# Performance work log

Hardware: AMD Instinct MI355X
Metric: run time of the kernel (lower is better)

## Reference

```python
import jax, jax.numpy as jnp
import numpy as np

B, N, M, LDIM, RDIM, AGG = 4, 512, 512, 512, 512, 256


def setup_inputs() -> dict:
    key = jax.random.key(0)
    ks = jax.random.split(key, 7)
    data = jax.random.normal(ks[0], (B, N, LDIM), dtype=jnp.float32)
    crit = jax.random.normal(ks[1], (B, M, RDIM), dtype=jnp.float32)
    Wl = jax.random.normal(ks[2], (LDIM, AGG), dtype=jnp.float32) / np.sqrt(LDIM)
    bl = jax.random.normal(ks[3], (AGG,), dtype=jnp.float32) * 0.01
    Wr = jax.random.normal(ks[4], (RDIM, AGG), dtype=jnp.float32) / np.sqrt(RDIM)
    br = jax.random.normal(ks[5], (AGG,), dtype=jnp.float32) * 0.01
    agg = jax.random.uniform(ks[6], (AGG,), dtype=jnp.float32, minval=-0.01, maxval=0.01)
    return {"data": data, "crit": crit, "Wl": Wl, "bl": bl, "Wr": Wr, "br": br, "agg": agg}


def reference(data, crit, Wl, bl, Wr, br, agg):
    # linear projections
    datalin = jnp.einsum('bnl,la->bna', data, Wl) + bl   # [B,N,A]
    critlin = jnp.einsum('bmr,ra->bma', crit, Wr) + br   # [B,M,A]
    # broadcast add -> tanh -> reduce with agg vector: [B,N,M]
    linsum = jnp.tanh(datalin[:, :, None, :] + critlin[:, None, :, :])  # [B,N,M,A]
    dists = jnp.einsum('bnma,a->bnm', linsum, agg)
    return dists
```

## Files before the change

### kernel.cpp

```cpp
#include <hip/hip_runtime.h>


#define A_DIM 256
#define K_DIM 512
#define NROWS 2048

typedef unsigned short ushort;
typedef __attribute__((ext_vector_type(4))) unsigned short us4;
typedef __attribute__((ext_vector_type(8))) unsigned short us8;
typedef __attribute__((ext_vector_type(8))) short short8;
typedef __attribute__((ext_vector_type(4))) float f32x4;

__device__ inline ushort f2bf(float x) {
    union { float f; unsigned u; } v; v.f = x;
    unsigned r = v.u + 0x7FFFu + ((v.u >> 16) & 1u);
    return (ushort)(r >> 16);
}
__device__ inline float bf2f(ushort h) {
    union { unsigned u; float f; } v; v.u = ((unsigned)h) << 16; return v.f;
}
__device__ inline unsigned pack2bf(float lo, float hi) {
    return (unsigned)f2bf(lo) | ((unsigned)f2bf(hi) << 16);
}

__global__ __launch_bounds__(256) void transpose_w_kernel(
    const float* __restrict__ Wl, const float* __restrict__ Wr,
    ushort* __restrict__ wt)
{
    __shared__ float tile[64][68];
    const int t   = threadIdx.x;
    const int bid = blockIdx.x;
    const int at  = bid & 3;
    const int kt  = (bid >> 2) & 7;
    const int src = bid >> 5;
    const int a0 = at * 64, k0 = kt * 64;
    const float* W = src ? Wr : Wl;
    ushort* out = wt + (size_t)src * (A_DIM * K_DIM);

    const int c4 = (t & 15) * 4;
    const int kr = t >> 4;
#pragma unroll
    for (int r = 0; r < 4; r++) {
        const int k = kr + r * 16;
        *(float4*)&tile[k][c4] = *(const float4*)(W + (size_t)(k0 + k) * A_DIM + a0 + c4);
    }
    __syncthreads();
    const int aL  = t & 63;
    const int ks0 = (t >> 6) * 16;
#pragma unroll
    for (int g = 0; g < 4; g++) {
        us4 o;
#pragma unroll
        for (int i = 0; i < 4; i++) o[i] = f2bf(tile[ks0 + g * 4 + i][aL]);
        *(us4*)(out + (size_t)(a0 + aL) * K_DIM + k0 + ks0 + g * 4) = o;
    }
}

__global__ __launch_bounds__(256) void proj_mfma_kernel(
    const float* __restrict__ data, const float* __restrict__ crit,
    const float* __restrict__ bl, const float* __restrict__ br,
    const ushort* __restrict__ wt, ushort* __restrict__ eplanes)
{
    __shared__ ushort Ws[64][264];

    const int t   = threadIdx.x;
    const int bid = blockIdx.x;
    const int ct  = bid & 3;
    const int rt  = bid >> 2;
    const int src = rt >> 6;
    const int lr0 = (rt & 63) * 32;
    const int c0  = ct * 64;

    const float* X    = src ? crit : data;
    const float* bias = src ? br : bl;
    const ushort* Wt  = wt + (size_t)src * (A_DIM * K_DIM);
    ushort* E = eplanes + (size_t)src * ((size_t)A_DIM * NROWS);

    const int lane = t & 63;
    const int wid  = t >> 6;
    const int wm   = wid >> 1, wn = wid & 1;
    const int quad = lane >> 4, l16 = lane & 15;

    const float* xrow = X + (size_t)(lr0 + wm * 16 + l16) * K_DIM + quad * 8;
    const int aloc0 = wn * 32 + l16;

    f32x4 acc0 = {0.f, 0.f, 0.f, 0.f}, acc1 = {0.f, 0.f, 0.f, 0.f};

    float4 pa = *(const float4*)(xrow);
    float4 pb = *(const float4*)(xrow + 4);

    for (int kc = 0; kc < 2; kc++) {
        __syncthreads();
        {
            const int a  = t & 63;
            const int ks = (t >> 6) * 64;
            const ushort* s = Wt + (size_t)(c0 + a) * K_DIM + kc * 256 + ks;
#pragma unroll
            for (int i = 0; i < 8; i++)
                *(us8*)&Ws[a][ks + i * 8] = *(const us8*)(s + i * 8);
        }
        __syncthreads();

#pragma unroll
        for (int ls = 0; ls < 8; ls++) {
            const int s = kc * 8 + ls;
            float4 ca = pa, cb = pb;
            if (s < 15) {
                pa = *(const float4*)(xrow + (s + 1) * 32);
                pb = *(const float4*)(xrow + (s + 1) * 32 + 4);
            }
            union { short8 s8; unsigned u[4]; } af;
            af.u[0] = pack2bf(ca.x, ca.y);
            af.u[1] = pack2bf(ca.z, ca.w);
            af.u[2] = pack2bf(cb.x, cb.y);
            af.u[3] = pack2bf(cb.z, cb.w);
            short8 b0 = *(const short8*)&Ws[aloc0     ][ls * 32 + quad * 8];
            short8 b1 = *(const short8*)&Ws[aloc0 + 16][ls * 32 + quad * 8];
            acc0 = __builtin_amdgcn_mfma_f32_16x16x32_bf16(af.s8, b0, acc0, 0, 0, 0);
            acc1 = __builtin_amdgcn_mfma_f32_16x16x32_bf16(af.s8, b1, acc1, 0, 0, 0);
        }
    }

    const float c2 = 2.8853900817779268f;
    const int a_col0 = c0 + wn * 32 + l16;
    const int a_col1 = a_col0 + 16;
    const int row0   = lr0 + wm * 16 + quad * 4;
    const float bv0 = bias[a_col0], bv1 = bias[a_col1];
    us4 e0, e1;
#pragma unroll
    for (int i = 0; i < 4; i++) {
        float v0 = (acc0[i] + bv0) * c2;
        float v1 = (acc1[i] + bv1) * c2;
        v0 = fminf(fmaxf(v0, -15.f), 15.f);
        v1 = fminf(fmaxf(v1, -15.f), 15.f);
        e0[i] = f2bf(__builtin_amdgcn_exp2f(v0));
        e1[i] = f2bf(__builtin_amdgcn_exp2f(v1));
    }
    *(us4*)(E + (size_t)a_col0 * NROWS + row0) = e0;
    *(us4*)(E + (size_t)a_col1 * NROWS + row0) = e1;
}

__global__ __launch_bounds__(512) void tanh_reduce_kernel(
    const ushort* __restrict__ eplanes, const float* __restrict__ agg,
    float* __restrict__ out)
{
    __shared__ __align__(16) float et [2][64][68];
    __shared__ __align__(16) float ect[2][64][68];
    __shared__ float aggs[256];

    const int t  = threadIdx.x;
    const int h  = t >> 8;
    const int u  = t & 255;
    const int m0 = blockIdx.x * 64;
    const int n0 = blockIdx.y * 64;
    const int b  = blockIdx.z;

    const size_t PLANE = (size_t)A_DIM * NROWS;
    const ushort* Ed = eplanes;
    const ushort* Ec = eplanes + PLANE;
    const int row_n = b * 512 + n0;
    const int row_m = b * 512 + m0;

    const int tx = u & 15;
    const int ty = u >> 4;

    if (t < 256) aggs[t] = 2.0f * agg[t];

    float acc[4][4];
#pragma unroll
    for (int i = 0; i < 4; i++)
#pragma unroll
        for (int j = 0; j < 4; j++) acc[i][j] = 0.f;
    float sagg = 0.f;

    const int aL = u >> 2;
    const int qd = u & 3;

    float (*eth)[68]  = et[h];
    float (*ecth)[68] = ect[h];

    for (int ch = 0; ch < 2; ch++) {
        const int a0 = h * 128 + ch * 64;
        __syncthreads();
#pragma unroll
        for (int r = 0; r < 4; r++) {
            const int seg = qd * 16 + r * 4;
            us4 d = *(const us4*)(Ed + (size_t)(a0 + aL) * NROWS + row_n + seg);
            us4 c = *(const us4*)(Ec + (size_t)(a0 + aL) * NROWS + row_m + seg);
            float4 ev, cv;
            ev.x = bf2f(d[0]); ev.y = bf2f(d[1]); ev.z = bf2f(d[2]); ev.w = bf2f(d[3]);
            cv.x = bf2f(c[0]); cv.y = bf2f(c[1]); cv.z = bf2f(c[2]); cv.w = bf2f(c[3]);
            *(float4*)&eth [aL][seg] = ev;
            *(float4*)&ecth[aL][seg] = cv;
        }
        __syncthreads();

        for (int p = 0; p < 32; p++) {
            const float2 ag = *(const float2*)&aggs[h * 128 + ch * 64 + p * 2];
            sagg += ag.x + ag.y;
            float4 e0 = *(const float4*)&eth [p * 2 + 0][ty * 4];
            float4 e1 = *(const float4*)&eth [p * 2 + 1][ty * 4];
            float4 f0 = *(const float4*)&ecth[p * 2 + 0][tx * 4];
            float4 f1 = *(const float4*)&ecth[p * 2 + 1][tx * 4];
            const float ea0[4] = {e0.x, e0.y, e0.z, e0.w};
            const float ea1[4] = {e1.x, e1.y, e1.z, e1.w};
            const float fa0[4] = {f0.x, f0.y, f0.z, f0.w};
            const float fa1[4] = {f1.x, f1.y, f1.z, f1.w};
#pragma unroll
            for (int i = 0; i < 4; i++)
#pragma unroll
                for (int j = 0; j < 4; j++) {
                    float q0 = fmaf(ea0[i], fa0[j], 1.f);
                    float q1 = fmaf(ea1[i], fa1[j], 1.f);
                    acc[i][j] = fmaf(fmaf(ag.x, q1, ag.y * q0),
                                     __builtin_amdgcn_rcpf(q0 * q1), acc[i][j]);
                }
        }
    }

    const float base = 0.5f * sagg;
    float* xb = (float*)ect;
    __syncthreads();
    if (h == 1) {
#pragma unroll
        for (int i = 0; i < 4; i++)
#pragma unroll
            for (int j = 0; j < 4; j++)
                xb[u * 17 + i * 4 + j] = base - acc[i][j];
    }
    __syncthreads();
    if (h == 0) {
#pragma unroll
        for (int i = 0; i < 4; i++) {
            float4 v;
            v.x = (base - acc[i][0]) + xb[u * 17 + i * 4 + 0];
            v.y = (base - acc[i][1]) + xb[u * 17 + i * 4 + 1];
            v.z = (base - acc[i][2]) + xb[u * 17 + i * 4 + 2];
            v.w = (base - acc[i][3]) + xb[u * 17 + i * 4 + 3];
            *(float4*)(out + ((size_t)(b * 512 + n0 + ty * 4 + i) * 512) + m0 + tx * 4) = v;
        }
    }
}

extern "C" void kernel_launch(void* const* d_in, const int* in_sizes, int n_in,
                              void* d_out, int out_size, void* d_ws, size_t ws_size,
                              hipStream_t stream) {
    const float* data = (const float*)d_in[0];
    const float* crit = (const float*)d_in[1];
    const float* Wl   = (const float*)d_in[2];
    const float* bl   = (const float*)d_in[3];
    const float* Wr   = (const float*)d_in[4];
    const float* br   = (const float*)d_in[5];
    const float* agg  = (const float*)d_in[6];
    float* out = (float*)d_out;

    ushort* ws16 = (ushort*)d_ws;
    ushort* eplanes = ws16;
    ushort* wt      = ws16 + 2 * (size_t)A_DIM * NROWS;

    transpose_w_kernel<<<dim3(64), 256, 0, stream>>>(Wl, Wr, wt);

    proj_mfma_kernel<<<dim3(512), 256, 0, stream>>>(data, crit, bl, br, wt, eplanes);

    tanh_reduce_kernel<<<dim3(8, 8, 4), 512, 0, stream>>>(eplanes, agg, out);
}
```

Baseline: 110.3 us.

## Group four tanh terms per reciprocal, packed FMA math, prefetch next chunk

The inner tanh-reduce loop now combines four aggregate dimensions into a single rational expression, so only one reciprocal is needed per four tanh terms instead of one per two, and uses packed two-wide FP32 FMAs. It also prefetches the second chunk's bf16 planes into registers while the first chunk is computed, and switches the output and workspace writes to nontemporal stores. Multiplying four (1+e*f) factors risks overflow or precision loss when the exponentials are large, and the extra prefetch registers may lower occupancy.

Measured after the change: 107.8 us. 1.02x faster.

```diff
diff --git a/kernel.cpp b/kernel.cpp
--- a/kernel.cpp
+++ b/kernel.cpp
@@ -10,6 +10,7 @@
 typedef __attribute__((ext_vector_type(8))) unsigned short us8;
 typedef __attribute__((ext_vector_type(8))) short short8;
 typedef __attribute__((ext_vector_type(4))) float f32x4;
+typedef __attribute__((ext_vector_type(2))) float f32x2;
 
 __device__ inline ushort f2bf(float x) {
     union { float f; unsigned u; } v; v.f = x;
@@ -21,6 +22,9 @@
 }
 __device__ inline unsigned pack2bf(float lo, float hi) {
     return (unsigned)f2bf(lo) | ((unsigned)f2bf(hi) << 16);
+}
+__device__ inline f32x2 fma2(f32x2 a, f32x2 b, f32x2 c) {
+    return __builtin_elementwise_fma(a, b, c);
 }
 
 __global__ __launch_bounds__(256) void transpose_w_kernel(
@@ -52,7 +56,7 @@
         us4 o;
 #pragma unroll
         for (int i = 0; i < 4; i++) o[i] = f2bf(tile[ks0 + g * 4 + i][aL]);
-        *(us4*)(out + (size_t)(a0 + aL) * K_DIM + k0 + ks0 + g * 4) = o;
+        __builtin_nontemporal_store(o, (us4*)(out + (size_t)(a0 + aL) * K_DIM + k0 + ks0 + g * 4));
     }
 }
 
@@ -136,8 +140,8 @@
         e0[i] = f2bf(__builtin_amdgcn_exp2f(v0));
         e1[i] = f2bf(__builtin_amdgcn_exp2f(v1));
     }
-    *(us4*)(E + (size_t)a_col0 * NROWS + row0) = e0;
-    *(us4*)(E + (size_t)a_col1 * NROWS + row0) = e1;
+    __builtin_nontemporal_store(e0, (us4*)(E + (size_t)a_col0 * NROWS + row0));
+    __builtin_nontemporal_store(e1, (us4*)(E + (size_t)a_col1 * NROWS + row0));
 }
 
 __global__ __launch_bounds__(512) void tanh_reduce_kernel(
@@ -146,7 +150,7 @@
 {
     __shared__ __align__(16) float et [2][64][68];
     __shared__ __align__(16) float ect[2][64][68];
-    __shared__ float aggs[256];
+    __shared__ __align__(16) float aggs[256];
 
     const int t  = threadIdx.x;
     const int h  = t >> 8;
@@ -166,11 +170,9 @@
 
     if (t < 256) aggs[t] = 2.0f * agg[t];
 
-    float acc[4][4];
-#pragma unroll
-    for (int i = 0; i < 4; i++)
-#pragma unroll
-        for (int j = 0; j < 4; j++) acc[i][j] = 0.f;
+    f32x2 acc2[4][2];
+#pragma unroll
+    for (int i = 0; i < 4; i++) { acc2[i][0] = (f32x2)0.f; acc2[i][1] = (f32x2)0.f; }
     float sagg = 0.f;
 
     const int aL = u >> 2;
@@ -179,41 +181,67 @@
     float (*eth)[68]  = et[h];
     float (*ecth)[68] = ect[h];
 
+    us4 pn[4], pm[4];
+#pragma unroll
+    for (int r = 0; r < 4; r++) {
+        const size_t base = (size_t)(h * 128 + aL) * NROWS;
+        pn[r] = *(const us4*)(Ed + base + row_n + qd * 16 + r * 4);
+        pm[r] = *(const us4*)(Ec + base + row_m + qd * 16 + r * 4);
+    }
+
     for (int ch = 0; ch < 2; ch++) {
-        const int a0 = h * 128 + ch * 64;
         __syncthreads();
 #pragma unroll
         for (int r = 0; r < 4; r++) {
-            const int seg = qd * 16 + r * 4;
-            us4 d = *(const us4*)(Ed + (size_t)(a0 + aL) * NROWS + row_n + seg);
-            us4 c = *(const us4*)(Ec + (size_t)(a0 + aL) * NROWS + row_m + seg);
             float4 ev, cv;
-            ev.x = bf2f(d[0]); ev.y = bf2f(d[1]); ev.z = bf2f(d[2]); ev.w = bf2f(d[3]);
-            cv.x = bf2f(c[0]); cv.y = bf2f(c[1]); cv.z = bf2f(c[2]); cv.w = bf2f(c[3]);
-            *(float4*)&eth [aL][seg] = ev;
-            *(float4*)&ecth[aL][seg] = cv;
-        }
-        __syncthreads();
-
-        for (int p = 0; p < 32; p++) {
-            const float2 ag = *(const float2*)&aggs[h * 128 + ch * 64 + p * 2];
-            sagg += ag.x + ag.y;
-            float4 e0 = *(const float4*)&eth [p * 2 + 0][ty * 4];
-            float4 e1 = *(const float4*)&eth [p * 2 + 1][ty * 4];
-            float4 f0 = *(const float4*)&ecth[p * 2 + 0][tx * 4];
-            float4 f1 = *(const float4*)&ecth[p * 2 + 1][tx * 4];
-            const float ea0[4] = {e0.x, e0.y, e0.z, e0.w};
-            const float ea1[4] = {e1.x, e1.y, e1.z, e1.w};
-            const float fa0[4] = {f0.x, f0.y, f0.z, f0.w};
-            const float fa1[4] = {f1.x, f1.y, f1.z, f1.w};
+            ev.x = bf2f(pn[r][0]); ev.y = bf2f(pn[r][1]);
+            ev.z = bf2f(pn[r][2]); ev.w = bf2f(pn[r][3]);
+            cv.x = bf2f(pm[r][0]); cv.y = bf2f(pm[r][1]);
+            cv.z = bf2f(pm[r][2]); cv.w = bf2f(pm[r][3]);
+            *(float4*)&eth [aL][qd * 16 + r * 4] = ev;
+            *(float4*)&ecth[aL][qd * 16 + r * 4] = cv;
+        }
+        __syncthreads();
+        if (ch == 0) {
+            const size_t base = (size_t)(h * 128 + 64 + aL) * NROWS;
+#pragma unroll
+            for (int r = 0; r < 4; r++) {
+                pn[r] = *(const us4*)(Ed + base + row_n + qd * 16 + r * 4);
+                pm[r] = *(const us4*)(Ec + base + row_m + qd * 16 + r * 4);
+            }
+        }
+
+        for (int qg = 0; qg < 16; qg++) {
+            const float4 ag = *(const float4*)&aggs[h * 128 + ch * 64 + qg * 4];
+            sagg += (ag.x + ag.y) + (ag.z + ag.w);
+            float  en[4][4];
+            f32x2  fm[4][2];
+#pragma unroll
+            for (int v = 0; v < 4; v++) {
+                float4 e4 = *(const float4*)&eth [qg * 4 + v][ty * 4];
+                float4 f4 = *(const float4*)&ecth[qg * 4 + v][tx * 4];
+                en[v][0] = e4.x; en[v][1] = e4.y; en[v][2] = e4.z; en[v][3] = e4.w;
+                fm[v][0] = f32x2{f4.x, f4.y};
+                fm[v][1] = f32x2{f4.z, f4.w};
+            }
 #pragma unroll
             for (int i = 0; i < 4; i++)
 #pragma unroll
-                for (int j = 0; j < 4; j++) {
-                    float q0 = fmaf(ea0[i], fa0[j], 1.f);
-                    float q1 = fmaf(ea1[i], fa1[j], 1.f);
-                    acc[i][j] = fmaf(fmaf(ag.x, q1, ag.y * q0),
-                                     __builtin_amdgcn_rcpf(q0 * q1), acc[i][j]);
+                for (int jp = 0; jp < 2; jp++) {
+                    const f32x2 one = (f32x2)1.f;
+                    f32x2 q0 = fma2((f32x2)en[0][i], fm[0][jp], one);
+                    f32x2 q1 = fma2((f32x2)en[1][i], fm[1][jp], one);
+                    f32x2 q2 = fma2((f32x2)en[2][i], fm[2][jp], one);
+                    f32x2 q3 = fma2((f32x2)en[3][i], fm[3][jp], one);
+                    f32x2 q01 = q0 * q1, q23 = q2 * q3;
+                    f32x2 n01 = fma2((f32x2)ag.x, q1, (f32x2)ag.y * q0);
+                    f32x2 n23 = fma2((f32x2)ag.z, q3, (f32x2)ag.w * q2);
+                    f32x2 N   = fma2(n01, q23, n23 * q01);
+                    f32x2 D   = q01 * q23;
+                    f32x2 r;
+                    r.x = __builtin_amdgcn_rcpf(D.x);
+                    r.y = __builtin_amdgcn_rcpf(D.y);
+                    acc2[i][jp] = fma2(N, r, acc2[i][jp]);
                 }
         }
     }
@@ -225,19 +253,22 @@
 #pragma unroll
         for (int i = 0; i < 4; i++)
 #pragma unroll
-            for (int j = 0; j < 4; j++)
-                xb[u * 17 + i * 4 + j] = base - acc[i][j];
+            for (int jp = 0; jp < 2; jp++) {
+                xb[u * 17 + i * 4 + jp * 2 + 0] = base - acc2[i][jp].x;
+                xb[u * 17 + i * 4 + jp * 2 + 1] = base - acc2[i][jp].y;
+            }
     }
     __syncthreads();
     if (h == 0) {
 #pragma unroll
         for (int i = 0; i < 4; i++) {
-            float4 v;
-            v.x = (base - acc[i][0]) + xb[u * 17 + i * 4 + 0];
-            v.y = (base - acc[i][1]) + xb[u * 17 + i * 4 + 1];
-            v.z = (base - acc[i][2]) + xb[u * 17 + i * 4 + 2];
-            v.w = (base - acc[i][3]) + xb[u * 17 + i * 4 + 3];
-            *(float4*)(out + ((size_t)(b * 512 + n0 + ty * 4 + i) * 512) + m0 + tx * 4) = v;
+            f32x4 v;
+            v.x = (base - acc2[i][0].x) + xb[u * 17 + i * 4 + 0];
+            v.y = (base - acc2[i][0].y) + xb[u * 17 + i * 4 + 1];
+            v.z = (base - acc2[i][1].x) + xb[u * 17 + i * 4 + 2];
+            v.w = (base - acc2[i][1].y) + xb[u * 17 + i * 4 + 3];
+            __builtin_nontemporal_store(v,
+                (f32x4*)(out + ((size_t)(b * 512 + n0 + ty * 4 + i) * 512) + m0 + tx * 4));
         }
     }
 }
@@ -254,9 +285,8 @@
     const float* agg  = (const float*)d_in[6];
     float* out = (float*)d_out;
 
-    ushort* ws16 = (ushort*)d_ws;
-    ushort* eplanes = ws16;
-    ushort* wt      = ws16 + 2 * (size_t)A_DIM * NROWS;
+    ushort* eplanes = (ushort*)d_ws;
+    ushort* wt      = eplanes + 2 * (size_t)A_DIM * NROWS;
 
     transpose_w_kernel<<<dim3(64), 256, 0, stream>>>(Wl, Wr, wt);
 
```
